# Kernel optimization log

Measured on AMD Instinct MI355X. Metric: run time of the kernel, lower is better.

The kernel has to match this reference:

```python
import jax, jax.numpy as jnp
from jax import lax
import numpy as np

B, T, I, H, O = 2048, 256, 88, 64, 13


def _lstm_layer(xs, w_ih, w_hh, b):
    # xs: [T, B, in], w_ih: [4H, in], w_hh: [4H, H], b: [4H] (b_ih + b_hh)
    Bb = xs.shape[1]
    Hh = w_hh.shape[1]

    def step(carry, x_t):
        h, c = carry
        g = x_t @ w_ih.T + h @ w_hh.T + b  # [B, 4H]
        i, f, gg, o = jnp.split(g, 4, axis=-1)  # PyTorch gate order: i, f, g, o
        i = jax.nn.sigmoid(i)
        f = jax.nn.sigmoid(f)
        gg = jnp.tanh(gg)
        o = jax.nn.sigmoid(o)
        c = f * c + i * gg
        h = o * jnp.tanh(c)
        return (h, c), h

    init = (jnp.zeros((Bb, Hh), xs.dtype), jnp.zeros((Bb, Hh), xs.dtype))
    (h_last, _), ys = lax.scan(step, init, xs)
    return ys, h_last


def setup_inputs() -> dict:
    key = jax.random.key(0)
    ks = jax.random.split(key, 12)
    s = lambda fan: 1.0 / np.sqrt(H)  # PyTorch LSTM init scale 1/sqrt(H)
    u = lambda k, shape: jax.random.uniform(k, shape, jnp.float32, -s(H), s(H))
    return {
        "x": jax.random.normal(ks[0], (B, T, I), jnp.float32),
        "w_ih0": u(ks[1], (4 * H, I)),
        "w_hh0": u(ks[2], (4 * H, H)),
        "b_ih0": u(ks[3], (4 * H,)),
        "b_hh0": u(ks[4], (4 * H,)),
        "w_ih1": u(ks[5], (4 * H, H)),
        "w_hh1": u(ks[6], (4 * H, H)),
        "b_ih1": u(ks[7], (4 * H,)),
        "b_hh1": u(ks[8], (4 * H,)),
        "fc_w": u(ks[9], (O, H)),
        "fc_b": u(ks[10], (O,)),
    }


def reference(x, w_ih0, w_hh0, b_ih0, b_hh0, w_ih1, w_hh1, b_ih1, b_hh1, fc_w, fc_b):
    xs = jnp.transpose(x, (1, 0, 2))  # [T, B, I]
    ys1, _ = _lstm_layer(xs, w_ih0, w_hh0, b_ih0 + b_hh0)  # [T, B, H]
    # inter-layer dropout and head dropout are identity in eval mode
    _, h_last = _lstm_layer(ys1, w_ih1, w_hh1, b_ih1 + b_hh1)  # [B, H]
    return h_last @ fc_w.T + fc_b  # [B, O]
```

## Files before the change

### kernel.cpp

```cpp
#include <hip/hip_runtime.h>
#include <hip/hip_bf16.h>


#define B_ 2048
#define T_ 256
#define I_ 88
#define H_ 64
#define O_ 13
#define G4H 256
#define TC 32
#define CR (B_ * TC)
#define NCK (T_ / TC)

__device__ __align__(16) float g_gpre[(size_t)CR * G4H];
__device__ __align__(16) float g_ysc[(size_t)CR * H_];
__device__ __align__(16) float g_wp[(I_ + H_) * G4H];
__device__ float g_h[2][B_ * H_];
__device__ float g_c[2][B_ * H_];

__device__ __forceinline__ float sigmoid_f(float v) {
    return 1.f / (1.f + __expf(-v));
}
__device__ __forceinline__ float tanh_f(float v) {
    return 1.f - 2.f / (__expf(2.f * v) + 1.f);
}

__global__ void prep_weights(const float* __restrict__ wih0, const float* __restrict__ wih1) {
    int id = blockIdx.x * blockDim.x + threadIdx.x;
    const int S0 = I_ * G4H;
    const int S1 = S0 + H_ * G4H;
    if (id >= S1) return;
    const float* src;
    int base, K;
    if (id < S0) { base = 0;  src = wih0; K = I_; }
    else         { base = S0; src = wih1; K = H_; }
    int loc = id - base;
    int k   = loc >> 8;
    int col = loc & 255;
    int hh  = col >> 2;
    int g   = col & 3;
    g_wp[id] = src[(g * H_ + hh) * K + k];
}

__global__ __launch_bounds__(256, 1) void gemm_l0(const float* __restrict__ x, int ck) {
    extern __shared__ __align__(16) float wl[];
    const int tid = threadIdx.x;
    for (int i = tid; i < (I_ * G4H) / 4; i += 256)
        ((float4*)wl)[i] = ((const float4*)g_wp)[i];
    __syncthreads();

    const int j  = tid & 63;
    const int wv = __builtin_amdgcn_readfirstlane(tid >> 6);

    for (int p = 0; p < 8; ++p) {
        const int qb = (blockIdx.x << 8) + (p << 5) + (wv << 3);
        const float* xr[8];
#pragma unroll
        for (int m = 0; m < 8; ++m) {
            const int q = qb + m;
            const long in_row = (long)(q & (B_ - 1)) * T_ + ck * TC + (q >> 11);
            xr[m] = x + (size_t)in_row * I_;
        }
        float4 acc[8];
#pragma unroll
        for (int m = 0; m < 8; ++m) acc[m] = make_float4(0.f, 0.f, 0.f, 0.f);

#pragma unroll 2
        for (int k = 0; k < I_; ++k) {
            const float4 w4 = *(const float4*)&wl[(k << 8) + (j << 2)];
#pragma unroll
            for (int m = 0; m < 8; ++m) {
                const float xv = xr[m][k];
                acc[m].x += w4.x * xv; acc[m].y += w4.y * xv;
                acc[m].z += w4.z * xv; acc[m].w += w4.w * xv;
            }
        }
#pragma unroll
        for (int m = 0; m < 8; ++m) {
            float* o = g_gpre + (size_t)(qb + m) * G4H + j;
            o[0]   = acc[m].x;
            o[64]  = acc[m].y;
            o[128] = acc[m].z;
            o[192] = acc[m].w;
        }
    }
}

__global__ __launch_bounds__(256, 1) void gemm_l1() {
    extern __shared__ __align__(16) float wl[];
    const int tid = threadIdx.x;
    for (int i = tid; i < (H_ * G4H) / 4; i += 256)
        ((float4*)wl)[i] = ((const float4*)(g_wp + I_ * G4H))[i];
    __syncthreads();

    const int j  = tid & 63;
    const int wv = __builtin_amdgcn_readfirstlane(tid >> 6);

    for (int p = 0; p < 8; ++p) {
        const int qb = (blockIdx.x << 8) + (p << 5) + (wv << 3);
        const float* xr[8];
#pragma unroll
        for (int m = 0; m < 8; ++m) xr[m] = g_ysc + (size_t)(qb + m) * H_;

        float4 acc[8];
#pragma unroll
        for (int m = 0; m < 8; ++m) acc[m] = make_float4(0.f, 0.f, 0.f, 0.f);

#pragma unroll 2
        for (int k = 0; k < H_; ++k) {
            const float4 w4 = *(const float4*)&wl[(k << 8) + (j << 2)];
#pragma unroll
            for (int m = 0; m < 8; ++m) {
                const float xv = xr[m][k];
                acc[m].x += w4.x * xv; acc[m].y += w4.y * xv;
                acc[m].z += w4.z * xv; acc[m].w += w4.w * xv;
            }
        }
#pragma unroll
        for (int m = 0; m < 8; ++m) {
            float* o = g_gpre + (size_t)(qb + m) * G4H + j;
            o[0]   = acc[m].x;
            o[64]  = acc[m].y;
            o[128] = acc[m].z;
            o[192] = acc[m].w;
        }
    }
}

__global__ __launch_bounds__(256, 1) void lstm_rec(const float* __restrict__ whh,
                                                   const float* __restrict__ bih,
                                                   const float* __restrict__ bhh,
                                                   const int layer, const int ck,
                                                   const float* __restrict__ fcw,
                                                   const float* __restrict__ fcb,
                                                   float* __restrict__ out) {
    __shared__ __align__(16) float hl[H_];
    __shared__ float xch[4][H_];

    const int tid = threadIdx.x;
    const int j   = tid & 63;
    const int g   = __builtin_amdgcn_readfirstlane(tid >> 6);
    const int r   = blockIdx.x;

    float4 w[16];
    const float* wrow = whh + (size_t)(g * H_ + j) * H_;
#pragma unroll
    for (int kk = 0; kk < 16; ++kk) w[kk] = ((const float4*)wrow)[kk];

    const float bias = bih[g * H_ + j] + bhh[g * H_ + j];
    if (tid < H_) hl[tid] = ck ? g_h[layer][r * H_ + tid] : 0.f;
    float c = 0.f;
    if (g == 0 && ck) c = g_c[layer][r * H_ + j];

    const float* gp = g_gpre + (size_t)r * G4H + g * H_ + j;
    float gpv = gp[0];
    __syncthreads();

    for (int tl = 0; tl < TC; ++tl) {
        float a0 = 0.f, a1 = 0.f, a2 = 0.f, a3 = 0.f;
#pragma unroll
        for (int kk = 0; kk < 16; kk += 4) {
            const float4 h0 = *(const float4*)&hl[(kk + 0) << 2];
            a0 += w[kk + 0].x * h0.x; a0 += w[kk + 0].y * h0.y;
            a0 += w[kk + 0].z * h0.z; a0 += w[kk + 0].w * h0.w;
            const float4 h1 = *(const float4*)&hl[(kk + 1) << 2];
            a1 += w[kk + 1].x * h1.x; a1 += w[kk + 1].y * h1.y;
            a1 += w[kk + 1].z * h1.z; a1 += w[kk + 1].w * h1.w;
            const float4 h2 = *(const float4*)&hl[(kk + 2) << 2];
            a2 += w[kk + 2].x * h2.x; a2 += w[kk + 2].y * h2.y;
            a2 += w[kk + 2].z * h2.z; a2 += w[kk + 2].w * h2.w;
            const float4 h3 = *(const float4*)&hl[(kk + 3) << 2];
            a3 += w[kk + 3].x * h3.x; a3 += w[kk + 3].y * h3.y;
            a3 += w[kk + 3].z * h3.z; a3 += w[kk + 3].w * h3.w;
        }
        const float pre = bias + gpv + ((a0 + a1) + (a2 + a3));
        if (tl + 1 < TC) gpv = gp[(size_t)(tl + 1) * B_ * G4H];

        const float act = (g == 2) ? tanh_f(pre) : sigmoid_f(pre);
        xch[g][j] = act;
        __syncthreads();

        if (g == 0) {
            const float iv = xch[0][j], fv = xch[1][j], gv = xch[2][j], ov = xch[3][j];
            c = fv * c + iv * gv;
            const float h = ov * tanh_f(c);
            hl[j] = h;
            if (layer == 0) g_ysc[((size_t)tl * B_ + r) * H_ + j] = h;
        }
        __syncthreads();
    }

    if (g == 0) {
        g_h[layer][r * H_ + j] = hl[j];
        g_c[layer][r * H_ + j] = c;
        if (layer == 1 && ck == NCK - 1 && j < O_) {
            float s = fcb[j];
            const float* wr = fcw + j * H_;
#pragma unroll
            for (int k = 0; k < H_; ++k) s += hl[k] * wr[k];
            out[(size_t)r * O_ + j] = s;
        }
    }
}

extern "C" void kernel_launch(void* const* d_in, const int* in_sizes, int n_in,
                              void* d_out, int out_size, void* d_ws, size_t ws_size,
                              hipStream_t stream) {
    const float* x    = (const float*)d_in[0];
    const float* wih0 = (const float*)d_in[1];
    const float* whh0 = (const float*)d_in[2];
    const float* bih0 = (const float*)d_in[3];
    const float* bhh0 = (const float*)d_in[4];
    const float* wih1 = (const float*)d_in[5];
    const float* whh1 = (const float*)d_in[6];
    const float* bih1 = (const float*)d_in[7];
    const float* bhh1 = (const float*)d_in[8];
    const float* fcw  = (const float*)d_in[9];
    const float* fcb  = (const float*)d_in[10];
    float* out = (float*)d_out;

    const int lds0 = I_ * G4H * 4;
    const int lds1 = H_ * G4H * 4;
    hipFuncSetAttribute((const void*)gemm_l0, hipFuncAttributeMaxDynamicSharedMemorySize, lds0);
    hipFuncSetAttribute((const void*)gemm_l1, hipFuncAttributeMaxDynamicSharedMemorySize, lds1);

    prep_weights<<<dim3(152), dim3(256), 0, stream>>>(wih0, wih1);

    for (int ck = 0; ck < NCK; ++ck) {
        gemm_l0<<<dim3(CR / 256), dim3(256), lds0, stream>>>(x, ck);
        lstm_rec<<<dim3(B_), dim3(256), 0, stream>>>(whh0, bih0, bhh0, 0, ck, fcw, fcb, out);
        gemm_l1<<<dim3(CR / 256), dim3(256), lds1, stream>>>();
        lstm_rec<<<dim3(B_), dim3(256), 0, stream>>>(whh1, bih1, bhh1, 1, ck, fcw, fcb, out);
    }
}
```

Baseline: 2.453 ms.

## Process four batch rows per block in recurrent LSTM kernel

Each recurrent block now handles four batch rows instead of one, reusing the register-resident W_hh weights across the four rows. The h state is stored interleaved so one float4 LDS read feeds four accumulators, and all four waves now do the cell update for their own row instead of only wave 0. This cuts weight loads from global memory and the block count by four, and spreads the serial cell-update work across waves. In exchange there are fewer blocks in flight (512), more registers per thread, and four activations per thread per step.

```diff
diff --git a/kernel.cpp b/kernel.cpp
--- a/kernel.cpp
+++ b/kernel.cpp
@@ -11,6 +11,7 @@
 #define TC 32
 #define CR (B_ * TC)
 #define NCK (T_ / TC)
+#define NBR 4
 
 __device__ __align__(16) float g_gpre[(size_t)CR * G4H];
 __device__ __align__(16) float g_ysc[(size_t)CR * H_];
@@ -134,13 +135,13 @@
                                                    const float* __restrict__ fcw,
                                                    const float* __restrict__ fcb,
                                                    float* __restrict__ out) {
-    __shared__ __align__(16) float hl[H_];
-    __shared__ float xch[4][H_];
+    __shared__ __align__(16) float hl[H_][NBR];
+    __shared__ float xch[NBR][4][H_];
 
     const int tid = threadIdx.x;
     const int j   = tid & 63;
-    const int g   = __builtin_amdgcn_readfirstlane(tid >> 6);
-    const int r   = blockIdx.x;
+    const int g   = tid >> 6;
+    const int r0  = blockIdx.x * NBR;
 
     float4 w[16];
     const float* wrow = whh + (size_t)(g * H_ + j) * H_;
@@ -148,58 +149,61 @@
     for (int kk = 0; kk < 16; ++kk) w[kk] = ((const float4*)wrow)[kk];
 
     const float bias = bih[g * H_ + j] + bhh[g * H_ + j];
-    if (tid < H_) hl[tid] = ck ? g_h[layer][r * H_ + tid] : 0.f;
-    float c = 0.f;
-    if (g == 0 && ck) c = g_c[layer][r * H_ + j];
-
-    const float* gp = g_gpre + (size_t)r * G4H + g * H_ + j;
-    float gpv = gp[0];
+
+    ((float*)hl)[tid] = ck ? g_h[layer][(size_t)(r0 + (tid & 3)) * H_ + (tid >> 2)] : 0.f;
+    float c = ck ? g_c[layer][(size_t)(r0 + g) * H_ + j] : 0.f;
+
+    const float* gp = g_gpre + (size_t)r0 * G4H + g * H_ + j;
+    float p0 = gp[0 * G4H], p1 = gp[1 * G4H], p2 = gp[2 * G4H], p3 = gp[3 * G4H];
     __syncthreads();
 
     for (int tl = 0; tl < TC; ++tl) {
-        float a0 = 0.f, a1 = 0.f, a2 = 0.f, a3 = 0.f;
-#pragma unroll
-        for (int kk = 0; kk < 16; kk += 4) {
-            const float4 h0 = *(const float4*)&hl[(kk + 0) << 2];
-            a0 += w[kk + 0].x * h0.x; a0 += w[kk + 0].y * h0.y;
-            a0 += w[kk + 0].z * h0.z; a0 += w[kk + 0].w * h0.w;
-            const float4 h1 = *(const float4*)&hl[(kk + 1) << 2];
-            a1 += w[kk + 1].x * h1.x; a1 += w[kk + 1].y * h1.y;
-            a1 += w[kk + 1].z * h1.z; a1 += w[kk + 1].w * h1.w;
-            const float4 h2 = *(const float4*)&hl[(kk + 2) << 2];
-            a2 += w[kk + 2].x * h2.x; a2 += w[kk + 2].y * h2.y;
-            a2 += w[kk + 2].z * h2.z; a2 += w[kk + 2].w * h2.w;
-            const float4 h3 = *(const float4*)&hl[(kk + 3) << 2];
-            a3 += w[kk + 3].x * h3.x; a3 += w[kk + 3].y * h3.y;
-            a3 += w[kk + 3].z * h3.z; a3 += w[kk + 3].w * h3.w;
-        }
-        const float pre = bias + gpv + ((a0 + a1) + (a2 + a3));
-        if (tl + 1 < TC) gpv = gp[(size_t)(tl + 1) * B_ * G4H];
-
-        const float act = (g == 2) ? tanh_f(pre) : sigmoid_f(pre);
-        xch[g][j] = act;
+        float a0 = bias + p0, a1 = bias + p1, a2 = bias + p2, a3 = bias + p3;
+#pragma unroll
+        for (int kk = 0; kk < 16; ++kk) {
+            const float4 wv4 = w[kk];
+            const float4 h0 = *(const float4*)&hl[(kk << 2) + 0][0];
+            a0 += wv4.x * h0.x; a1 += wv4.x * h0.y; a2 += wv4.x * h0.z; a3 += wv4.x * h0.w;
+            const float4 h1 = *(const float4*)&hl[(kk << 2) + 1][0];
+            a0 += wv4.y * h1.x; a1 += wv4.y * h1.y; a2 += wv4.y * h1.z; a3 += wv4.y * h1.w;
+            const float4 h2 = *(const float4*)&hl[(kk << 2) + 2][0];
+            a0 += wv4.z * h2.x; a1 += wv4.z * h2.y; a2 += wv4.z * h2.z; a3 += wv4.z * h2.w;
+            const float4 h3 = *(const float4*)&hl[(kk << 2) + 3][0];
+            a0 += wv4.w * h3.x; a1 += wv4.w * h3.y; a2 += wv4.w * h3.z; a3 += wv4.w * h3.w;
+        }
+        if (tl + 1 < TC) {
+            const float* gn = gp + (size_t)(tl + 1) * B_ * G4H;
+            p0 = gn[0 * G4H]; p1 = gn[1 * G4H]; p2 = gn[2 * G4H]; p3 = gn[3 * G4H];
+        }
+        if (g == 2) {
+            xch[0][g][j] = tanh_f(a0); xch[1][g][j] = tanh_f(a1);
+            xch[2][g][j] = tanh_f(a2); xch[3][g][j] = tanh_f(a3);
+        } else {
+            xch[0][g][j] = sigmoid_f(a0); xch[1][g][j] = sigmoid_f(a1);
+            xch[2][g][j] = sigmoid_f(a2); xch[3][g][j] = sigmoid_f(a3);
+        }
         __syncthreads();
 
-        if (g == 0) {
-            const float iv = xch[0][j], fv = xch[1][j], gv = xch[2][j], ov = xch[3][j];
+        {
+            const float iv = xch[g][0][j], fv = xch[g][1][j];
+            const float gv = xch[g][2][j], ov = xch[g][3][j];
             c = fv * c + iv * gv;
             const float h = ov * tanh_f(c);
-            hl[j] = h;
-            if (layer == 0) g_ysc[((size_t)tl * B_ + r) * H_ + j] = h;
+            hl[j][g] = h;
+            if (layer == 0) g_ysc[((size_t)tl * B_ + (r0 + g)) * H_ + j] = h;
         }
         __syncthreads();
     }
 
-    if (g == 0) {
-        g_h[layer][r * H_ + j] = hl[j];
-        g_c[layer][r * H_ + j] = c;
-        if (layer == 1 && ck == NCK - 1 && j < O_) {
-            float s = fcb[j];
-            const float* wr = fcw + j * H_;
-#pragma unroll
-            for (int k = 0; k < H_; ++k) s += hl[k] * wr[k];
-            out[(size_t)r * O_ + j] = s;
-        }
+    g_h[layer][(size_t)(r0 + g) * H_ + j] = hl[j][g];
+    g_c[layer][(size_t)(r0 + g) * H_ + j] = c;
+
+    if (layer == 1 && ck == NCK - 1 && j < O_) {
+        float s = fcb[j];
+        const float* wr = fcw + j * H_;
+#pragma unroll
+        for (int k = 0; k < H_; ++k) s += hl[k][g] * wr[k];
+        out[(size_t)(r0 + g) * O_ + j] = s;
     }
 }
 
@@ -228,8 +232,8 @@
 
     for (int ck = 0; ck < NCK; ++ck) {
         gemm_l0<<<dim3(CR / 256), dim3(256), lds0, stream>>>(x, ck);
-        lstm_rec<<<dim3(B_), dim3(256), 0, stream>>>(whh0, bih0, bhh0, 0, ck, fcw, fcb, out);
+        lstm_rec<<<dim3(B_ / NBR), dim3(256), 0, stream>>>(whh0, bih0, bhh0, 0, ck, fcw, fcb, out);
         gemm_l1<<<dim3(CR / 256), dim3(256), lds1, stream>>>();
-        lstm_rec<<<dim3(B_), dim3(256), 0, stream>>>(whh1, bih1, bhh1, 1, ck, fcw, fcb, out);
-    }
-}
+        lstm_rec<<<dim3(B_ / NBR), dim3(256), 0, stream>>>(whh1, bih1, bhh1, 1, ck, fcw, fcb, out);
+    }
+}
```

Measured after the change: 2.416 ms. No clear change (-1.5%).
